# Kernel optimization log

Measured on AMD Instinct MI355X. Metric: run time of the kernel, lower is better.

Reference implementation:

```python
import jax, jax.numpy as jnp
import numpy as np

# ShapeNet category -> contiguous segment range (16 categories, 50 segments)
SEG_LENS = np.array([4, 2, 2, 4, 4, 3, 3, 2, 4, 2, 6, 2, 3, 3, 3, 3], dtype=np.int32)
SHIFTS = np.concatenate([[0], np.cumsum(SEG_LENS)[:-1]]).astype(np.int32)
NUM_CAT = 16
IN_F = 256
MAX_SEG_COUNT = 6   # max len(seg) over categories
MAX_SEG = 49        # max segment id
N_PTS = 32768
BN_EPS = 1e-5


def setup_inputs() -> dict:
    key = jax.random.key(0)
    k1, k2, k3, k4 = jax.random.split(key, 4)
    features = jax.random.normal(k1, (N_PTS, IN_F), dtype=jnp.float32)
    W1 = jax.random.normal(k2, (IN_F, NUM_CAT * IN_F), dtype=jnp.float32) * (1.0 / np.sqrt(IN_F))
    gamma = jnp.ones((NUM_CAT * IN_F,), dtype=jnp.float32)
    beta = jnp.zeros((NUM_CAT * IN_F,), dtype=jnp.float32)
    Wc = jax.random.normal(k3, (NUM_CAT, IN_F, MAX_SEG_COUNT), dtype=jnp.float32) * (1.0 / np.sqrt(IN_F))
    bias = jnp.zeros((MAX_SEG_COUNT,), dtype=jnp.float32)
    cats = jax.random.randint(k4, (N_PTS,), 0, NUM_CAT, dtype=jnp.int32)
    return {
        "features": features, "W1": W1, "gamma": gamma, "beta": beta,
        "Wc": Wc, "bias": bias, "cats": cats,
        "shifts": jnp.asarray(SHIFTS), "seg_lens": jnp.asarray(SEG_LENS),
    }


def reference(features, W1, gamma, beta, Wc, bias, cats, shifts, seg_lens):
    N, F = features.shape
    C, _, S = Wc.shape
    # channel_rasing: Linear(bias=False) -> BatchNorm1d (batch stats) -> LeakyReLU(0.2)
    x = features @ W1                              # [N, C*F]
    mu = x.mean(axis=0)
    var = x.var(axis=0)                            # biased, as BatchNorm
    x = (x - mu) * jax.lax.rsqrt(var + BN_EPS) * gamma + beta
    x = jnp.where(x >= 0, x, 0.2 * x)              # LeakyReLU(0.2); Dropout = identity (eval)
    # UnaryConv: per-category matmul + shared bias -> [C, N, S]
    x = x.reshape(N, C, F)
    feats = jnp.einsum('ncf,cfs->cns', x, Wc) + bias
    # gather the assigned category's logits per point -> [N, S]
    logits = feats[cats, jnp.arange(N)]
    lsm = jax.nn.log_softmax(logits, axis=-1)
    # scatter (expressed as gather) into per-category segment ranges -> [N, MAX_SEG+1]
    sh = shifts[cats]                              # [N]
    ln = seg_lens[cats]                            # [N]
    k = jnp.arange(MAX_SEG + 1, dtype=jnp.int32)   # [50]
    j = k[None, :] - sh[:, None]                   # [N, 50]
    valid = (j >= 0) & (j < ln[:, None])
    jc = jnp.clip(j, 0, S - 1)
    out = jnp.where(valid, jnp.take_along_axis(lsm, jc, axis=1), 0.0)
    return out
```

## Files before the change

kernel.cpp:

```cpp
#include <hip/hip_runtime.h>
#include <hip/hip_bf16.h>
#include <math.h>

#define N_PTS 32768
#define IN_F  256
#define NUM_CAT 16
#define CF    4096
#define NSEG  6
#define OUTK  50
#define BN_EPS 1e-5f

typedef unsigned short u16;
typedef __attribute__((ext_vector_type(8))) short bf16x8;
typedef __attribute__((ext_vector_type(4))) float f32x4;
typedef __attribute__((ext_vector_type(8))) unsigned short u16x8;

#define OFF_G     0u
#define OFF_FBAR  65536u
#define OFF_SCALE 65792u
#define OFF_SHIFT 69888u
#define OFF_INT   73984u
#define OFF_FB    106832u
#define OFF_FBT   4301136u
#define OFF_W1T   8495440u
#define OFF_GP    9019728u
#define IO_COUNTS 0
#define IO_CATOFF 16
#define IO_TILEST 33
#define IO_NTILES 50
#define IO_CURSOR 51
#define IO_ORDER  67

__device__ __forceinline__ void gload_lds16(const void* g, void* l) {
    __builtin_amdgcn_global_load_lds(
        (const __attribute__((address_space(1))) void*)g,
        (__attribute__((address_space(3))) void*)l,
        16, 0, 0);
}
__device__ __forceinline__ u16 f2bf(float f) {
    unsigned int u = __float_as_uint(f);
    return (u16)((u + 0x7FFF + ((u >> 16) & 1)) >> 16);
}
__device__ __forceinline__ float bf2f(u16 h) {
    return __uint_as_float((unsigned int)h << 16);
}

__global__ __launch_bounds__(256) void k0_cvt(const float* __restrict__ F,
                                              u16* __restrict__ Fb,
                                              u16* __restrict__ FbT) {
    const int pb = blockIdx.x >> 2, fb = blockIdx.x & 3;
    const int p0 = pb * 64, f0 = fb * 64;
    const int tid = threadIdx.x;
    __shared__ u16 T[64][72];
    {
        int p = tid >> 2, fq = tid & 3;
        const float* src = &F[(size_t)(p0 + p) * IN_F + f0 + fq * 16];
        u16x8 o0, o1;
        float4 v0 = *(const float4*)&src[0];
        float4 v1 = *(const float4*)&src[4];
        float4 v2 = *(const float4*)&src[8];
        float4 v3 = *(const float4*)&src[12];
        o0[0]=f2bf(v0.x); o0[1]=f2bf(v0.y); o0[2]=f2bf(v0.z); o0[3]=f2bf(v0.w);
        o0[4]=f2bf(v1.x); o0[5]=f2bf(v1.y); o0[6]=f2bf(v1.z); o0[7]=f2bf(v1.w);
        o1[0]=f2bf(v2.x); o1[1]=f2bf(v2.y); o1[2]=f2bf(v2.z); o1[3]=f2bf(v2.w);
        o1[4]=f2bf(v3.x); o1[5]=f2bf(v3.y); o1[6]=f2bf(v3.z); o1[7]=f2bf(v3.w);
        u16* dst = &Fb[(size_t)(p0 + p) * IN_F + f0 + fq * 16];
        *(u16x8*)dst = o0; *(u16x8*)&dst[8] = o1;
        *(u16x8*)&T[p][fq * 16] = o0; *(u16x8*)&T[p][fq * 16 + 8] = o1;
    }
    __syncthreads();
    {
        int f = tid >> 2, pq = tid & 3;
        u16x8 a0, a1;
#pragma unroll
        for (int m = 0; m < 8; m++) { a0[m] = T[pq*16 + m][f]; a1[m] = T[pq*16 + 8 + m][f]; }
        u16* dst = &FbT[(size_t)(f0 + f) * N_PTS + p0 + pq * 16];
        *(u16x8*)dst = a0; *(u16x8*)&dst[8] = a1;
    }
}

__global__ __launch_bounds__(256) void k0b_w1t(const float* __restrict__ W1,
                                               u16* __restrict__ W1T) {
    __shared__ u16 T[64][65];
    const int kb = blockIdx.x & 3, jb = blockIdx.x >> 2;
    const int tid = threadIdx.x;
    {
        int kk = tid >> 2, j4 = (tid & 3) * 16;
        const float* src = &W1[(size_t)(kb * 64 + kk) * CF + jb * 64 + j4];
#pragma unroll
        for (int q = 0; q < 4; q++) {
            float4 v = *(const float4*)&src[q * 4];
            T[kk][j4 + q * 4 + 0] = f2bf(v.x); T[kk][j4 + q * 4 + 1] = f2bf(v.y);
            T[kk][j4 + q * 4 + 2] = f2bf(v.z); T[kk][j4 + q * 4 + 3] = f2bf(v.w);
        }
    }
    __syncthreads();
    {
        int jj = tid >> 2, ks = (tid & 3) * 16;
        int c = jb >> 2, n = (jb & 3) * 64 + jj;
        u16* dst = &W1T[((size_t)(c * 256 + n)) * 256 + kb * 64 + ks];
        u16x8 o0, o1;
#pragma unroll
        for (int m = 0; m < 8; m++) { o0[m] = T[ks + m][jj]; o1[m] = T[ks + 8 + m][jj]; }
        *(u16x8*)dst = o0;
        *(u16x8*)&dst[8] = o1;
    }
}

__global__ __launch_bounds__(256) void k1_gram(const u16* __restrict__ FbT,
                                               float* __restrict__ ws,
                                               int nchunk, int Kc) {
    const int TI[10] = {0,0,0,0,1,1,1,2,2,3};
    const int TJ[10] = {0,1,2,3,1,2,3,2,3,3};
    const int t = blockIdx.x % 10, chunk = blockIdx.x / 10;
    const int i0 = TI[t] * 64, j0 = TJ[t] * 64;
    const int r0 = chunk * Kc;
    const int tid = threadIdx.x;
    const int wv = tid >> 6, ln = tid & 63, g = ln >> 4, r16 = ln & 15;
    __shared__ __align__(16) u16 SA[2][4096];
    __shared__ __align__(16) u16 SB[2][4096];

    const int q0 = wv * 2, q1 = wv * 2 + 1;
    const int u_a = ((q0 * 64 + ln) & 7), row_a = (q0 * 64 + ln) >> 3;
    const int u_b = ((q1 * 64 + ln) & 7), row_b = (q1 * 64 + ln) >> 3;
    const int ka = ((u_a ^ (row_a & 7)) << 3), kb2 = ((u_b ^ (row_b & 7)) << 3);

    f32x4 acc[4];
#pragma unroll
    for (int nt = 0; nt < 4; nt++)
#pragma unroll
        for (int i = 0; i < 4; i++) acc[nt][i] = 0.f;

    const int nslab = Kc >> 6;
#define K1_STAGE(s, b)                                                              \
    {   int p0s = r0 + (s) * 64;                                                    \
        gload_lds16(FbT + (size_t)(i0 + row_a) * N_PTS + p0s + ka,                  \
                    (char*)SA[b] + q0 * 1024);                                      \
        gload_lds16(FbT + (size_t)(i0 + row_b) * N_PTS + p0s + kb2,                 \
                    (char*)SA[b] + q1 * 1024);                                      \
        gload_lds16(FbT + (size_t)(j0 + row_a) * N_PTS + p0s + ka,                  \
                    (char*)SB[b] + q0 * 1024);                                      \
        gload_lds16(FbT + (size_t)(j0 + row_b) * N_PTS + p0s + kb2,                 \
                    (char*)SB[b] + q1 * 1024);                                      \
    }

    K1_STAGE(0, 0);
    __syncthreads();
    for (int s = 0; s < nslab; s++) {
        const int b = s & 1;
        if (s + 1 < nslab) K1_STAGE(s + 1, b ^ 1);
#pragma unroll
        for (int ks = 0; ks < 2; ks++) {
            int ph = (ks * 4 + g) ^ (r16 & 7);
            bf16x8 a = *(const bf16x8*)((const char*)SA[b] + (wv * 16 + r16) * 128 + ph * 16);
#pragma unroll
            for (int nt = 0; nt < 4; nt++) {
                int nB = nt * 16 + r16;
                bf16x8 bb = *(const bf16x8*)((const char*)SB[b] + nB * 128 + ph * 16);
                acc[nt] = __builtin_amdgcn_mfma_f32_16x16x32_bf16(a, bb, acc[nt], 0, 0, 0);
            }
        }
        __syncthreads();
    }
    float* Gp = ws + OFF_GP + (size_t)chunk * 40960 + t * 4096;
#pragma unroll
    for (int nt = 0; nt < 4; nt++)
#pragma unroll
        for (int i = 0; i < 4; i++) {
            int row = wv * 16 + g * 4 + i, col = nt * 16 + r16;
            Gp[row * 64 + col] = acc[nt][i];
        }
}

__global__ __launch_bounds__(256) void k1b_colsum(const u16* __restrict__ FbT,
                                                  float* __restrict__ ws) {
    const int row = blockIdx.x, tid = threadIdx.x;
    const u16* r = FbT + (size_t)row * N_PTS;
    float s = 0.f;
    for (int i = tid * 8; i < N_PTS; i += 2048) {
        u16x8 v = *(const u16x8*)&r[i];
#pragma unroll
        for (int m = 0; m < 8; m++) s += bf2f(v[m]);
    }
#pragma unroll
    for (int off = 32; off >= 1; off >>= 1) s += __shfl_xor(s, off);
    __shared__ float ps[4];
    if ((tid & 63) == 0) ps[tid >> 6] = s;
    __syncthreads();
    if (tid == 0) ws[OFF_FBAR + row] = (ps[0] + ps[1] + ps[2] + ps[3]) * (1.0f / N_PTS);
    if (blockIdx.x == 0 && tid < 16) ((int*)(ws + OFF_INT))[IO_COUNTS + tid] = 0;
}

__global__ __launch_bounds__(256) void k2a_reduce(float* __restrict__ ws, int nchunk) {
    const int TI[10] = {0,0,0,0,1,1,1,2,2,3};
    const int TJ[10] = {0,1,2,3,1,2,3,2,3,3};
    const int e = blockIdx.x * 256 + threadIdx.x;
    const float* p = ws + OFF_GP + e;
    float s = 0.f;
#pragma unroll 8
    for (int c = 0; c < nchunk; c++) s += p[(size_t)c * 40960];
    int t = e >> 12, x = (e >> 6) & 63, y = e & 63;
    int a = TI[t] * 64 + x, b = TJ[t] * 64 + y;
    ws[OFF_G + a * 256 + b] = s;
    ws[OFF_G + b * 256 + a] = s;
}

__global__ __launch_bounds__(256) void k2b_stats(const float* __restrict__ W1,
                                                 const float* __restrict__ gamma,
                                                 const float* __restrict__ beta,
                                                 float* __restrict__ ws) {
    const int tid = threadIdx.x;
    const int j0 = blockIdx.x * 16;
    __shared__ __align__(16) float wl[16][256];
    __shared__ float pw[16][8];
#pragma unroll
    for (int q = 0; q < 4; q++) {
        float4 v = *(const float4*)&W1[(size_t)tid * CF + j0 + q * 4];
        wl[q * 4 + 0][tid] = v.x; wl[q * 4 + 1][tid] = v.y;
        wl[q * 4 + 2][tid] = v.z; wl[q * 4 + 3][tid] = v.w;
    }
    __syncthreads();
    float acc[16];
#pragma unroll
    for (int jj = 0; jj < 16; jj++) acc[jj] = 0.f;
    const float* G = ws + OFF_G;
    for (int b = 0; b < 256; b++) {
        float g = G[b * 256 + tid];
#pragma unroll
        for (int jj = 0; jj < 16; jj++) acc[jj] += g * wl[jj][b];
    }
    float fb = ws[OFF_FBAR + tid];
    const int lane = tid & 63, wave = tid >> 6;
#pragma unroll
    for (int jj = 0; jj < 16; jj++) {
        float v = wl[jj][tid] * acc[jj];
        float m = fb * wl[jj][tid];
#pragma unroll
        for (int off = 32; off >= 1; off >>= 1) {
            v += __shfl_xor(v, off);
            m += __shfl_xor(m, off);
        }
        if (lane == 0) { pw[jj][wave * 2] = v; pw[jj][wave * 2 + 1] = m; }
    }
    __syncthreads();
    if (tid < 16) {
        int jj = tid;
        float v = 0.f, m = 0.f;
        for (int w2 = 0; w2 < 4; w2++) { v += pw[jj][w2 * 2]; m += pw[jj][w2 * 2 + 1]; }
        float mu  = m;
        float var = v * (1.0f / N_PTS) - mu * mu;
        float sc  = gamma[j0 + jj] * rsqrtf(var + BN_EPS);
        float sh  = beta[j0 + jj] - mu * sc;
        ws[OFF_SCALE + j0 + jj] = sc;
        ws[OFF_SHIFT + j0 + jj] = sh;
    }
}

__global__ __launch_bounds__(256) void k3_hist(const int* __restrict__ cats,
                                               float* __restrict__ ws) {
    __shared__ int h[16];
    int tid = threadIdx.x;
    if (tid < 16) h[tid] = 0;
    __syncthreads();
    for (int n = blockIdx.x * 256 + tid; n < N_PTS; n += 64 * 256)
        atomicAdd(&h[cats[n]], 1);
    __syncthreads();
    int* wi = (int*)(ws + OFF_INT);
    if (tid < 16) atomicAdd(&wi[IO_COUNTS + tid], h[tid]);
}

__global__ void k4_prefix(float* __restrict__ ws) {
    int* wi = (int*)(ws + OFF_INT);
    if (threadIdx.x == 0) {
        int co = 0, ts = 0;
        wi[IO_CATOFF] = 0; wi[IO_TILEST] = 0;
        for (int c = 0; c < 16; c++) {
            int cnt = wi[IO_COUNTS + c];
            wi[IO_CURSOR + c] = co;
            co += cnt; ts += (cnt + 63) >> 6;
            wi[IO_CATOFF + c + 1] = co;
            wi[IO_TILEST + c + 1] = ts;
        }
        wi[IO_NTILES] = ts;
    }
}

__global__ __launch_bounds__(256) void k4b_scatter(const int* __restrict__ cats,
                                                   float* __restrict__ ws) {
    int* wi = (int*)(ws + OFF_INT);
    __shared__ int lh[16], lbase[16];
    const int tid = threadIdx.x;
    const int n0 = blockIdx.x * 512;
    if (tid < 16) lh[tid] = 0;
    __syncthreads();
    const int cA = cats[n0 + tid];
    const int cB = cats[n0 + 256 + tid];
    atomicAdd(&lh[cA], 1);
    atomicAdd(&lh[cB], 1);
    __syncthreads();
    if (tid < 16) lbase[tid] = atomicAdd(&wi[IO_CURSOR + tid], lh[tid]);
    __syncthreads();
    if (tid < 16) lh[tid] = 0;
    __syncthreads();
    int rA = atomicAdd(&lh[cA], 1);
    wi[IO_ORDER + lbase[cA] + rA] = n0 + tid;
    int rB = atomicAdd(&lh[cB], 1);
    wi[IO_ORDER + lbase[cB] + rB] = n0 + 256 + tid;
}

__global__ __launch_bounds__(256) void k5_mfma(const u16* __restrict__ Fb,
                                               const u16* __restrict__ W1T,
                                               const float* __restrict__ Wc,
                                               const float* __restrict__ bias,
                                               const int* __restrict__ shifts,
                                               const int* __restrict__ seg_lens,
                                               const float* __restrict__ ws,
                                               float* __restrict__ out) {
    const int* wi = (const int*)(ws + OFF_INT);
    const int t = blockIdx.x;
    if (t >= wi[IO_NTILES]) return;
    int c = 0;
    while (!(t >= wi[IO_TILEST + c] && t < wi[IO_TILEST + c + 1])) c++;
    const int lt = t - wi[IO_TILEST + c];
    const int base = wi[IO_CATOFF + c] + lt * 64;
    const int npts = min(64, wi[IO_COUNTS + c] - lt * 64);
    const int tid = threadIdx.x;
    const int wv = tid >> 6, ln = tid & 63;
    const int g = ln >> 4, r16 = ln & 15;

    __shared__ __align__(16) unsigned char U[32768];
    __shared__ float scl[256], shl[256], wcl[1536];
    __shared__ int plds[64];

    if (tid < 64) plds[tid] = wi[IO_ORDER + base + min(tid, npts - 1)];
    scl[tid] = ws[OFF_SCALE + c * 256 + tid];
    shl[tid] = ws[OFF_SHIFT + c * 256 + tid];
#pragma unroll
    for (int i = 0; i < 6; i++) wcl[tid + i * 256] = Wc[(size_t)c * 1536 + tid + i * 256];
    __syncthreads();

#pragma unroll
    for (int s = 0; s < 8; s++) {
        int flat = s * 256 + tid;
        int pt = flat >> 5, u = flat & 31;
        const u16* src = Fb + (size_t)plds[pt] * 256 + ((u ^ (pt & 7)) << 3);
        gload_lds16(src, U + (size_t)(s * 4 + wv) * 1024);
    }
    __syncthreads();

    const u16* W1Tc = W1T + (size_t)c * 65536;
    const u16* wp0 = W1Tc + (size_t)(wv * 64 +  0 + r16) * 256 + g * 8;
    const u16* wp1 = W1Tc + (size_t)(wv * 64 + 16 + r16) * 256 + g * 8;
    const u16* wp2 = W1Tc + (size_t)(wv * 64 + 32 + r16) * 256 + g * 8;
    const u16* wp3 = W1Tc + (size_t)(wv * 64 + 48 + r16) * 256 + g * 8;

    f32x4 acc[4][4];
#pragma unroll
    for (int mt = 0; mt < 4; mt++)
#pragma unroll
        for (int nt = 0; nt < 4; nt++)
#pragma unroll
            for (int i = 0; i < 4; i++) acc[mt][nt][i] = 0.f;

    bf16x8 bf[2][4];
    bf[0][0] = *(const bf16x8*)(wp0);
    bf[0][1] = *(const bf16x8*)(wp1);
    bf[0][2] = *(const bf16x8*)(wp2);
    bf[0][3] = *(const bf16x8*)(wp3);

#pragma unroll
    for (int kc = 0; kc < 8; kc++) {
        if (kc < 7) {
            bf[(kc + 1) & 1][0] = *(const bf16x8*)(wp0 + (kc + 1) * 32);
            bf[(kc + 1) & 1][1] = *(const bf16x8*)(wp1 + (kc + 1) * 32);
            bf[(kc + 1) & 1][2] = *(const bf16x8*)(wp2 + (kc + 1) * 32);
            bf[(kc + 1) & 1][3] = *(const bf16x8*)(wp3 + (kc + 1) * 32);
        }
        bf16x8 af[4];
#pragma unroll
        for (int mt = 0; mt < 4; mt++) {
            int row = mt * 16 + r16;
            int phys = (kc * 4 + g) ^ (row & 7);
            af[mt] = *(const bf16x8*)(U + (size_t)row * 512 + phys * 16);
        }
#pragma unroll
        for (int mt = 0; mt < 4; mt++)
#pragma unroll
            for (int nt = 0; nt < 4; nt++)
                acc[mt][nt] = __builtin_amdgcn_mfma_f32_16x16x32_bf16(
                    af[mt], bf[kc & 1][nt], acc[mt][nt], 0, 0, 0);
    }

    __syncthreads();
    float* red2 = (float*)U;
#pragma unroll
    for (int mt = 0; mt < 4; mt++)
#pragma unroll
        for (int i = 0; i < 4; i++) {
            float pl[6] = {0.f, 0.f, 0.f, 0.f, 0.f, 0.f};
#pragma unroll
            for (int nt = 0; nt < 4; nt++) {
                int col = wv * 64 + nt * 16 + r16;
                float x = acc[mt][nt][i] * scl[col] + shl[col];
                x = (x >= 0.f) ? x : 0.2f * x;
#pragma unroll
                for (int s = 0; s < 6; s++) pl[s] += x * wcl[col * 6 + s];
            }
#pragma unroll
            for (int s = 0; s < 6; s++) {
                pl[s] += __shfl_xor(pl[s], 1);
                pl[s] += __shfl_xor(pl[s], 2);
                pl[s] += __shfl_xor(pl[s], 4);
                pl[s] += __shfl_xor(pl[s], 8);
            }
            if (r16 == 0) {
                int pt = mt * 16 + g * 4 + i;
#pragma unroll
                for (int s = 0; s < 6; s++) red2[(pt * 4 + wv) * 6 + s] = pl[s];
            }
        }
    __syncthreads();

    if (tid < 64 && tid < npts) {
        float lg[6];
#pragma unroll
        for (int s = 0; s < 6; s++) lg[s] = bias[s];
#pragma unroll
        for (int w = 0; w < 4; w++)
#pragma unroll
            for (int s = 0; s < 6; s++) lg[s] += red2[(tid * 4 + w) * 6 + s];
        float mx = lg[0];
#pragma unroll
        for (int s = 1; s < 6; s++) mx = fmaxf(mx, lg[s]);
        float se = 0.f;
#pragma unroll
        for (int s = 0; s < 6; s++) se += expf(lg[s] - mx);
        float lse = mx + logf(se);
        const int pid = plds[tid];
        const int sh = shifts[c], ln2 = seg_lens[c];
        float* orow = out + (size_t)pid * OUTK;
        for (int k = 0; k < OUTK; k++) {
            int j = k - sh;
            orow[k] = (j >= 0 && j < ln2) ? (lg[j] - lse) : 0.f;
        }
    }
}

extern "C" void kernel_launch(void* const* d_in, const int* in_sizes, int n_in,
                              void* d_out, int out_size, void* d_ws, size_t ws_size,
                              hipStream_t stream) {
    const float* F      = (const float*)d_in[0];
    const float* W1     = (const float*)d_in[1];
    const float* gamma  = (const float*)d_in[2];
    const float* beta   = (const float*)d_in[3];
    const float* Wc     = (const float*)d_in[4];
    const float* bias   = (const float*)d_in[5];
    const int*  cats    = (const int*)d_in[6];
    const int*  shifts  = (const int*)d_in[7];
    const int*  seglens = (const int*)d_in[8];
    float* out = (float*)d_out;
    float* ws  = (float*)d_ws;
    u16* Fb  = (u16*)(ws + OFF_FB);
    u16* FbT = (u16*)(ws + OFF_FBT);
    u16* W1T = (u16*)(ws + OFF_W1T);

    int nchunk = 64;
    if (ws_size < ((size_t)OFF_GP + 40960ull * 64) * 4) nchunk = 32;
    if (ws_size < ((size_t)OFF_GP + 40960ull * 32) * 4) nchunk = 16;
    const int Kc = N_PTS / nchunk;

    hipLaunchKernelGGL(k0_cvt,      dim3(2048), dim3(256), 0, stream, F, Fb, FbT);
    hipLaunchKernelGGL(k0b_w1t,     dim3(256),  dim3(256), 0, stream, W1, W1T);
    hipLaunchKernelGGL(k1_gram,     dim3(10 * nchunk), dim3(256), 0, stream, FbT, ws, nchunk, Kc);
    hipLaunchKernelGGL(k1b_colsum,  dim3(256),  dim3(256), 0, stream, FbT, ws);
    hipLaunchKernelGGL(k2a_reduce,  dim3(160),  dim3(256), 0, stream, ws, nchunk);
    hipLaunchKernelGGL(k2b_stats,   dim3(256),  dim3(256), 0, stream, W1, gamma, beta, ws);
    hipLaunchKernelGGL(k3_hist,     dim3(64),   dim3(256), 0, stream, cats, ws);
    hipLaunchKernelGGL(k4_prefix,   dim3(1),    dim3(64),  0, stream, ws);
    hipLaunchKernelGGL(k4b_scatter, dim3(64),   dim3(256), 0, stream, cats, ws);
    hipLaunchKernelGGL(k5_mfma,     dim3(528),  dim3(256), 0, stream,
                       Fb, W1T, Wc, bias, shifts, seglens, ws, out);
}
```

Before: 115.3 us.

## Stage W1 tiles through LDS with double-buffered async loads in 512-thread GEMM

The main MFMA kernel moves to 512 threads (8 waves, each covering 32 output columns) and stages the category's W1 slice into swizzled LDS in four K-quarters. It double-buffers them with direct global-to-LDS loads and explicit vmcnt waits so that loads overlap compute. Tile-to-category lookup is precomputed in the prefix kernel as a packed table, replacing the per-block linear search. The cost is 96KB+ of LDS per block, which limits occupancy to about one block per CU, plus a larger cross-wave reduction.

```diff
diff --git a/kernel.cpp b/kernel.cpp
--- a/kernel.cpp
+++ b/kernel.cpp
@@ -20,16 +20,17 @@
 #define OFF_SCALE 65792u
 #define OFF_SHIFT 69888u
 #define OFF_INT   73984u
-#define OFF_FB    106832u
-#define OFF_FBT   4301136u
-#define OFF_W1T   8495440u
-#define OFF_GP    9019728u
+#define OFF_FB    107424u
+#define OFF_FBT   4301728u
+#define OFF_W1T   8496032u
+#define OFF_GP    9020320u
 #define IO_COUNTS 0
 #define IO_CATOFF 16
 #define IO_TILEST 33
 #define IO_NTILES 50
 #define IO_CURSOR 51
 #define IO_ORDER  67
+#define IO_TILECAT 32835
 
 __device__ __forceinline__ void gload_lds16(const void* g, void* l) {
     __builtin_amdgcn_global_load_lds(
@@ -277,7 +278,13 @@
         for (int c = 0; c < 16; c++) {
             int cnt = wi[IO_COUNTS + c];
             wi[IO_CURSOR + c] = co;
-            co += cnt; ts += (cnt + 63) >> 6;
+            int nt = (cnt + 63) >> 6;
+            for (int lt = 0; lt < nt; lt++) {
+                int npts = min(64, cnt - lt * 64);
+                int b = co + lt * 64;
+                wi[IO_TILECAT + ts + lt] = c | ((npts - 1) << 4) | (b << 10);
+            }
+            co += cnt; ts += nt;
             wi[IO_CATOFF + c + 1] = co;
             wi[IO_TILEST + c + 1] = ts;
         }
@@ -308,7 +315,7 @@
     wi[IO_ORDER + lbase[cB] + rB] = n0 + 256 + tid;
 }
 
-__global__ __launch_bounds__(256) void k5_mfma(const u16* __restrict__ Fb,
+__global__ __launch_bounds__(512) void k5_mfma(const u16* __restrict__ Fb,
                                                const u16* __restrict__ W1T,
                                                const float* __restrict__ Wc,
                                                const float* __restrict__ bias,
@@ -319,77 +326,101 @@
     const int* wi = (const int*)(ws + OFF_INT);
     const int t = blockIdx.x;
     if (t >= wi[IO_NTILES]) return;
-    int c = 0;
-    while (!(t >= wi[IO_TILEST + c] && t < wi[IO_TILEST + c + 1])) c++;
-    const int lt = t - wi[IO_TILEST + c];
-    const int base = wi[IO_CATOFF + c] + lt * 64;
-    const int npts = min(64, wi[IO_COUNTS + c] - lt * 64);
+    const unsigned info = (unsigned)wi[IO_TILECAT + t];
+    const int c    = info & 15;
+    const int npts = ((info >> 4) & 63) + 1;
+    const int base = info >> 10;
     const int tid = threadIdx.x;
     const int wv = tid >> 6, ln = tid & 63;
     const int g = ln >> 4, r16 = ln & 15;
 
-    __shared__ __align__(16) unsigned char U[32768];
+    __shared__ __align__(16) unsigned char U[98304];
     __shared__ float scl[256], shl[256], wcl[1536];
     __shared__ int plds[64];
 
     if (tid < 64) plds[tid] = wi[IO_ORDER + base + min(tid, npts - 1)];
-    scl[tid] = ws[OFF_SCALE + c * 256 + tid];
-    shl[tid] = ws[OFF_SHIFT + c * 256 + tid];
-#pragma unroll
-    for (int i = 0; i < 6; i++) wcl[tid + i * 256] = Wc[(size_t)c * 1536 + tid + i * 256];
-    __syncthreads();
-
-#pragma unroll
-    for (int s = 0; s < 8; s++) {
-        int flat = s * 256 + tid;
+    if (tid < 256) {
+        scl[tid] = ws[OFF_SCALE + c * 256 + tid];
+        shl[tid] = ws[OFF_SHIFT + c * 256 + tid];
+    }
+#pragma unroll
+    for (int i = 0; i < 3; i++) wcl[tid + i * 512] = Wc[(size_t)c * 1536 + tid + i * 512];
+    __syncthreads();
+
+    const u16* W1Tc = W1T + (size_t)c * 65536;
+
+#define STAGE_WQ(q, b)                                                             \
+    {                                                                              \
+        _Pragma("unroll")                                                          \
+        for (int i2 = 0; i2 < 4; i2++) {                                           \
+            int f = i2 * 64 + ln;                                                  \
+            int r = f >> 3, u = f & 7;                                             \
+            int n = wv * 32 + r;                                                   \
+            const u16* src = W1Tc + (size_t)n * 256 + (q) * 64 + ((u ^ (n & 7)) << 3); \
+            gload_lds16(src, U + 32768 + (b) * 32768 + wv * 4096 + i2 * 1024);     \
+        }                                                                          \
+    }
+
+    STAGE_WQ(0, 0);
+    STAGE_WQ(1, 1);
+#pragma unroll
+    for (int s = 0; s < 4; s++) {
+        int flat = (wv * 4 + s) * 64 + ln;
         int pt = flat >> 5, u = flat & 31;
         const u16* src = Fb + (size_t)plds[pt] * 256 + ((u ^ (pt & 7)) << 3);
-        gload_lds16(src, U + (size_t)(s * 4 + wv) * 1024);
-    }
-    __syncthreads();
-
-    const u16* W1Tc = W1T + (size_t)c * 65536;
-    const u16* wp0 = W1Tc + (size_t)(wv * 64 +  0 + r16) * 256 + g * 8;
-    const u16* wp1 = W1Tc + (size_t)(wv * 64 + 16 + r16) * 256 + g * 8;
-    const u16* wp2 = W1Tc + (size_t)(wv * 64 + 32 + r16) * 256 + g * 8;
-    const u16* wp3 = W1Tc + (size_t)(wv * 64 + 48 + r16) * 256 + g * 8;
-
-    f32x4 acc[4][4];
+        gload_lds16(src, U + (size_t)(wv * 4 + s) * 1024);
+    }
+    __syncthreads();
+
+    f32x4 acc[4][2];
 #pragma unroll
     for (int mt = 0; mt < 4; mt++)
 #pragma unroll
-        for (int nt = 0; nt < 4; nt++)
+        for (int nt = 0; nt < 2; nt++)
 #pragma unroll
             for (int i = 0; i < 4; i++) acc[mt][nt][i] = 0.f;
 
-    bf16x8 bf[2][4];
-    bf[0][0] = *(const bf16x8*)(wp0);
-    bf[0][1] = *(const bf16x8*)(wp1);
-    bf[0][2] = *(const bf16x8*)(wp2);
-    bf[0][3] = *(const bf16x8*)(wp3);
-
-#pragma unroll
-    for (int kc = 0; kc < 8; kc++) {
-        if (kc < 7) {
-            bf[(kc + 1) & 1][0] = *(const bf16x8*)(wp0 + (kc + 1) * 32);
-            bf[(kc + 1) & 1][1] = *(const bf16x8*)(wp1 + (kc + 1) * 32);
-            bf[(kc + 1) & 1][2] = *(const bf16x8*)(wp2 + (kc + 1) * 32);
-            bf[(kc + 1) & 1][3] = *(const bf16x8*)(wp3 + (kc + 1) * 32);
-        }
-        bf16x8 af[4];
-#pragma unroll
-        for (int mt = 0; mt < 4; mt++) {
-            int row = mt * 16 + r16;
-            int phys = (kc * 4 + g) ^ (row & 7);
-            af[mt] = *(const bf16x8*)(U + (size_t)row * 512 + phys * 16);
-        }
-#pragma unroll
-        for (int mt = 0; mt < 4; mt++)
-#pragma unroll
-            for (int nt = 0; nt < 4; nt++)
-                acc[mt][nt] = __builtin_amdgcn_mfma_f32_16x16x32_bf16(
-                    af[mt], bf[kc & 1][nt], acc[mt][nt], 0, 0, 0);
-    }
+#define COMP_Q(q, b)                                                               \
+    {                                                                              \
+        _Pragma("unroll")                                                          \
+        for (int h = 0; h < 2; h++) {                                              \
+            const int kc = (q) * 2 + h;                                            \
+            bf16x8 af[4], bfr[2];                                                  \
+            _Pragma("unroll")                                                      \
+            for (int mt = 0; mt < 4; mt++) {                                       \
+                int row = mt * 16 + r16;                                           \
+                int phys = (kc * 4 + g) ^ (row & 7);                               \
+                af[mt] = *(const bf16x8*)(U + (size_t)row * 512 + phys * 16);      \
+            }                                                                      \
+            _Pragma("unroll")                                                      \
+            for (int nt = 0; nt < 2; nt++) {                                       \
+                int n = wv * 32 + nt * 16 + r16;                                   \
+                int r = nt * 16 + r16;                                             \
+                int phys = (h * 4 + g) ^ (n & 7);                                  \
+                bfr[nt] = *(const bf16x8*)(U + 32768 + (b) * 32768                 \
+                                           + wv * 4096 + r * 128 + phys * 16);    \
+            }                                                                      \
+            _Pragma("unroll")                                                      \
+            for (int mt = 0; mt < 4; mt++)                                         \
+                _Pragma("unroll")                                                  \
+                for (int nt = 0; nt < 2; nt++)                                     \
+                    acc[mt][nt] = __builtin_amdgcn_mfma_f32_16x16x32_bf16(         \
+                        af[mt], bfr[nt], acc[mt][nt], 0, 0, 0);                    \
+        }                                                                          \
+    }
+
+    COMP_Q(0, 0);
+    __builtin_amdgcn_sched_barrier(0);
+    STAGE_WQ(2, 0);
+    COMP_Q(1, 1);
+    __builtin_amdgcn_sched_barrier(0);
+    STAGE_WQ(3, 1);
+    asm volatile("s_waitcnt vmcnt(4)" ::: "memory");
+    __builtin_amdgcn_sched_barrier(0);
+    COMP_Q(2, 0);
+    asm volatile("s_waitcnt vmcnt(0)" ::: "memory");
+    __builtin_amdgcn_sched_barrier(0);
+    COMP_Q(3, 1);
 
     __syncthreads();
     float* red2 = (float*)U;
@@ -399,8 +430,8 @@
         for (int i = 0; i < 4; i++) {
             float pl[6] = {0.f, 0.f, 0.f, 0.f, 0.f, 0.f};
 #pragma unroll
-            for (int nt = 0; nt < 4; nt++) {
-                int col = wv * 64 + nt * 16 + r16;
+            for (int nt = 0; nt < 2; nt++) {
+                int col = wv * 32 + nt * 16 + r16;
                 float x = acc[mt][nt][i] * scl[col] + shl[col];
                 x = (x >= 0.f) ? x : 0.2f * x;
 #pragma unroll
@@ -416,7 +447,7 @@
             if (r16 == 0) {
                 int pt = mt * 16 + g * 4 + i;
 #pragma unroll
-                for (int s = 0; s < 6; s++) red2[(pt * 4 + wv) * 6 + s] = pl[s];
+                for (int s = 0; s < 6; s++) red2[(pt * 8 + wv) * 6 + s] = pl[s];
             }
         }
     __syncthreads();
@@ -426,9 +457,9 @@
 #pragma unroll
         for (int s = 0; s < 6; s++) lg[s] = bias[s];
 #pragma unroll
-        for (int w = 0; w < 4; w++)
-#pragma unroll
-            for (int s = 0; s < 6; s++) lg[s] += red2[(tid * 4 + w) * 6 + s];
+        for (int w = 0; w < 8; w++)
+#pragma unroll
+            for (int s = 0; s < 6; s++) lg[s] += red2[(tid * 8 + w) * 6 + s];
         float mx = lg[0];
 #pragma unroll
         for (int s = 1; s < 6; s++) mx = fmaxf(mx, lg[s]);
@@ -478,6 +509,6 @@
     hipLaunchKernelGGL(k3_hist,     dim3(64),   dim3(256), 0, stream, cats, ws);
     hipLaunchKernelGGL(k4_prefix,   dim3(1),    dim3(64),  0, stream, ws);
     hipLaunchKernelGGL(k4b_scatter, dim3(64),   dim3(256), 0, stream, cats, ws);
-    hipLaunchKernelGGL(k5_mfma,     dim3(528),  dim3(256), 0, stream,
+    hipLaunchKernelGGL(k5_mfma,     dim3(528),  dim3(512), 0, stream,
                        Fb, W1T, Wc, bias, shifts, seglens, ws, out);
 }
```

New measurement: 151.0 us. 1.31x slower.

## Stage per-category W1 slice in LDS and stream 128-point tiles in chunks

Applied to the files above, without the earlier changes.

The main MFMA kernel now loads the whole 256x256 bf16 W1 slice for a category into LDS (128 KB) once per block. It then streams 128 points in 16-point double-buffered chunks with 512 threads, instead of reading W1 from global memory for every 64-point tile. Tile-to-category lookup moves into a precomputed packed table built by the prefix kernel, and the output is written cooperatively. The stats kernel processes 32 columns per block. This halves the number of W1 reads but uses very large LDS per block, so only one block fits per CU, and it adds a sync per chunk.

```diff
diff --git a/kernel.cpp b/kernel.cpp
--- a/kernel.cpp
+++ b/kernel.cpp
@@ -20,16 +20,17 @@
 #define OFF_SCALE 65792u
 #define OFF_SHIFT 69888u
 #define OFF_INT   73984u
-#define OFF_FB    106832u
-#define OFF_FBT   4301136u
-#define OFF_W1T   8495440u
-#define OFF_GP    9019728u
+#define OFF_FB    107424u
+#define OFF_FBT   4301728u
+#define OFF_W1T   8496032u
+#define OFF_GP    9020320u
 #define IO_COUNTS 0
 #define IO_CATOFF 16
 #define IO_TILEST 33
 #define IO_NTILES 50
 #define IO_CURSOR 51
 #define IO_ORDER  67
+#define IO_TILECAT 32835
 
 __device__ __forceinline__ void gload_lds16(const void* g, void* l) {
     __builtin_amdgcn_global_load_lds(
@@ -210,29 +211,29 @@
                                                  const float* __restrict__ beta,
                                                  float* __restrict__ ws) {
     const int tid = threadIdx.x;
-    const int j0 = blockIdx.x * 16;
-    __shared__ __align__(16) float wl[16][256];
-    __shared__ float pw[16][8];
-#pragma unroll
-    for (int q = 0; q < 4; q++) {
+    const int j0 = blockIdx.x * 32;
+    __shared__ __align__(16) float wl[32][256];
+    __shared__ float pw[32][8];
+#pragma unroll
+    for (int q = 0; q < 8; q++) {
         float4 v = *(const float4*)&W1[(size_t)tid * CF + j0 + q * 4];
         wl[q * 4 + 0][tid] = v.x; wl[q * 4 + 1][tid] = v.y;
         wl[q * 4 + 2][tid] = v.z; wl[q * 4 + 3][tid] = v.w;
     }
     __syncthreads();
-    float acc[16];
-#pragma unroll
-    for (int jj = 0; jj < 16; jj++) acc[jj] = 0.f;
+    float acc[32];
+#pragma unroll
+    for (int jj = 0; jj < 32; jj++) acc[jj] = 0.f;
     const float* G = ws + OFF_G;
     for (int b = 0; b < 256; b++) {
         float g = G[b * 256 + tid];
 #pragma unroll
-        for (int jj = 0; jj < 16; jj++) acc[jj] += g * wl[jj][b];
+        for (int jj = 0; jj < 32; jj++) acc[jj] += g * wl[jj][b];
     }
     float fb = ws[OFF_FBAR + tid];
     const int lane = tid & 63, wave = tid >> 6;
 #pragma unroll
-    for (int jj = 0; jj < 16; jj++) {
+    for (int jj = 0; jj < 32; jj++) {
         float v = wl[jj][tid] * acc[jj];
         float m = fb * wl[jj][tid];
 #pragma unroll
@@ -243,7 +244,7 @@
         if (lane == 0) { pw[jj][wave * 2] = v; pw[jj][wave * 2 + 1] = m; }
     }
     __syncthreads();
-    if (tid < 16) {
+    if (tid < 32) {
         int jj = tid;
         float v = 0.f, m = 0.f;
         for (int w2 = 0; w2 < 4; w2++) { v += pw[jj][w2 * 2]; m += pw[jj][w2 * 2 + 1]; }
@@ -277,7 +278,13 @@
         for (int c = 0; c < 16; c++) {
             int cnt = wi[IO_COUNTS + c];
             wi[IO_CURSOR + c] = co;
-            co += cnt; ts += (cnt + 63) >> 6;
+            int nt = (cnt + 127) >> 7;
+            for (int lt = 0; lt < nt; lt++) {
+                int npts = min(128, cnt - lt * 128);
+                int b = co + lt * 128;
+                wi[IO_TILECAT + ts + lt] = c | ((npts - 1) << 4) | (b << 11);
+            }
+            co += cnt; ts += nt;
             wi[IO_CATOFF + c + 1] = co;
             wi[IO_TILEST + c + 1] = ts;
         }
@@ -308,7 +315,7 @@
     wi[IO_ORDER + lbase[cB] + rB] = n0 + 256 + tid;
 }
 
-__global__ __launch_bounds__(256) void k5_mfma(const u16* __restrict__ Fb,
+__global__ __launch_bounds__(512) void k5_mfma(const u16* __restrict__ Fb,
                                                const u16* __restrict__ W1T,
                                                const float* __restrict__ Wc,
                                                const float* __restrict__ bias,
@@ -319,129 +326,122 @@
     const int* wi = (const int*)(ws + OFF_INT);
     const int t = blockIdx.x;
     if (t >= wi[IO_NTILES]) return;
-    int c = 0;
-    while (!(t >= wi[IO_TILEST + c] && t < wi[IO_TILEST + c + 1])) c++;
-    const int lt = t - wi[IO_TILEST + c];
-    const int base = wi[IO_CATOFF + c] + lt * 64;
-    const int npts = min(64, wi[IO_COUNTS + c] - lt * 64);
+    const unsigned info = (unsigned)wi[IO_TILECAT + t];
+    const int c    = info & 15;
+    const int npts = ((info >> 4) & 127) + 1;
+    const int base = info >> 11;
     const int tid = threadIdx.x;
     const int wv = tid >> 6, ln = tid & 63;
     const int g = ln >> 4, r16 = ln & 15;
 
-    __shared__ __align__(16) unsigned char U[32768];
-    __shared__ float scl[256], shl[256], wcl[1536];
-    __shared__ int plds[64];
-
-    if (tid < 64) plds[tid] = wi[IO_ORDER + base + min(tid, npts - 1)];
-    scl[tid] = ws[OFF_SCALE + c * 256 + tid];
-    shl[tid] = ws[OFF_SHIFT + c * 256 + tid];
-#pragma unroll
-    for (int i = 0; i < 6; i++) wcl[tid + i * 256] = Wc[(size_t)c * 1536 + tid + i * 256];
-    __syncthreads();
-
-#pragma unroll
-    for (int s = 0; s < 8; s++) {
-        int flat = s * 256 + tid;
-        int pt = flat >> 5, u = flat & 31;
-        const u16* src = Fb + (size_t)plds[pt] * 256 + ((u ^ (pt & 7)) << 3);
-        gload_lds16(src, U + (size_t)(s * 4 + wv) * 1024);
-    }
-    __syncthreads();
+    __shared__ __align__(16) u16 Wl[65536];
+    __shared__ __align__(16) u16 Fl[2][4096];
+    __shared__ float red[16][8][6];
+    __shared__ int plds[128];
+
+    if (tid < 128) plds[tid] = wi[IO_ORDER + base + min(tid, npts - 1)];
 
     const u16* W1Tc = W1T + (size_t)c * 65536;
-    const u16* wp0 = W1Tc + (size_t)(wv * 64 +  0 + r16) * 256 + g * 8;
-    const u16* wp1 = W1Tc + (size_t)(wv * 64 + 16 + r16) * 256 + g * 8;
-    const u16* wp2 = W1Tc + (size_t)(wv * 64 + 32 + r16) * 256 + g * 8;
-    const u16* wp3 = W1Tc + (size_t)(wv * 64 + 48 + r16) * 256 + g * 8;
-
-    f32x4 acc[4][4];
-#pragma unroll
-    for (int mt = 0; mt < 4; mt++)
-#pragma unroll
-        for (int nt = 0; nt < 4; nt++)
-#pragma unroll
-            for (int i = 0; i < 4; i++) acc[mt][nt][i] = 0.f;
-
-    bf16x8 bf[2][4];
-    bf[0][0] = *(const bf16x8*)(wp0);
-    bf[0][1] = *(const bf16x8*)(wp1);
-    bf[0][2] = *(const bf16x8*)(wp2);
-    bf[0][3] = *(const bf16x8*)(wp3);
-
-#pragma unroll
-    for (int kc = 0; kc < 8; kc++) {
-        if (kc < 7) {
-            bf[(kc + 1) & 1][0] = *(const bf16x8*)(wp0 + (kc + 1) * 32);
-            bf[(kc + 1) & 1][1] = *(const bf16x8*)(wp1 + (kc + 1) * 32);
-            bf[(kc + 1) & 1][2] = *(const bf16x8*)(wp2 + (kc + 1) * 32);
-            bf[(kc + 1) & 1][3] = *(const bf16x8*)(wp3 + (kc + 1) * 32);
-        }
-        bf16x8 af[4];
-#pragma unroll
-        for (int mt = 0; mt < 4; mt++) {
-            int row = mt * 16 + r16;
-            int phys = (kc * 4 + g) ^ (row & 7);
-            af[mt] = *(const bf16x8*)(U + (size_t)row * 512 + phys * 16);
-        }
-#pragma unroll
-        for (int mt = 0; mt < 4; mt++)
-#pragma unroll
-            for (int nt = 0; nt < 4; nt++)
-                acc[mt][nt] = __builtin_amdgcn_mfma_f32_16x16x32_bf16(
-                    af[mt], bf[kc & 1][nt], acc[mt][nt], 0, 0, 0);
-    }
-
-    __syncthreads();
-    float* red2 = (float*)U;
-#pragma unroll
-    for (int mt = 0; mt < 4; mt++)
+#pragma unroll
+    for (int i = 0; i < 16; i++) {
+        int flat = i * 512 + tid;
+        int n = flat >> 5, u = flat & 31;
+        const u16* src = W1Tc + (size_t)n * 256 + ((u ^ (n & 7)) << 3);
+        gload_lds16(src, (char*)Wl + i * 8192 + wv * 1024);
+    }
+
+    const int col0 = wv * 32 + r16, col1 = col0 + 16;
+    const float sc0 = ws[OFF_SCALE + c * 256 + col0];
+    const float sc1 = ws[OFF_SCALE + c * 256 + col1];
+    const float sh0 = ws[OFF_SHIFT + c * 256 + col0];
+    const float sh1 = ws[OFF_SHIFT + c * 256 + col1];
+    float wc0[6], wc1[6];
+#pragma unroll
+    for (int s = 0; s < 6; s++) {
+        wc0[s] = Wc[(size_t)c * 1536 + col0 * 6 + s];
+        wc1[s] = Wc[(size_t)c * 1536 + col1 * 6 + s];
+    }
+    const float biasj = ((tid & 7) < 6) ? bias[tid & 7] : 0.f;
+    const int shc = shifts[c], lnc = seg_lens[c];
+
+    __syncthreads();
+
+    const int fpt = tid >> 5, fu = tid & 31;
+    u16x8 pf = *(const u16x8*)(Fb + (size_t)plds[fpt] * 256 + fu * 8);
+    const int fdst = fpt * 256 + ((fu ^ (fpt & 7)) << 3);
+    const int r7 = r16 & 7;
+
+    for (int ck = 0; ck < 8; ck++) {
+        const int cur = ck & 1;
+        *(u16x8*)(Fl[cur] + fdst) = pf;
+        __syncthreads();
+        if (ck < 7)
+            pf = *(const u16x8*)(Fb + (size_t)plds[(ck + 1) * 16 + fpt] * 256 + fu * 8);
+
+        f32x4 acc0 = {0.f, 0.f, 0.f, 0.f}, acc1 = {0.f, 0.f, 0.f, 0.f};
+#pragma unroll
+        for (int kc = 0; kc < 8; kc++) {
+            const int ph = ((kc * 4 + g) ^ r7) * 16;
+            bf16x8 af = *(const bf16x8*)((const char*)Fl[cur] + r16 * 512 + ph);
+            bf16x8 b0 = *(const bf16x8*)((const char*)Wl + col0 * 512 + ph);
+            bf16x8 b1 = *(const bf16x8*)((const char*)Wl + col1 * 512 + ph);
+            acc0 = __builtin_amdgcn_mfma_f32_16x16x32_bf16(af, b0, acc0, 0, 0, 0);
+            acc1 = __builtin_amdgcn_mfma_f32_16x16x32_bf16(af, b1, acc1, 0, 0, 0);
+        }
+
+        float pl[4][6];
 #pragma unroll
         for (int i = 0; i < 4; i++) {
-            float pl[6] = {0.f, 0.f, 0.f, 0.f, 0.f, 0.f};
-#pragma unroll
-            for (int nt = 0; nt < 4; nt++) {
-                int col = wv * 64 + nt * 16 + r16;
-                float x = acc[mt][nt][i] * scl[col] + shl[col];
-                x = (x >= 0.f) ? x : 0.2f * x;
-#pragma unroll
-                for (int s = 0; s < 6; s++) pl[s] += x * wcl[col * 6 + s];
+            float x0 = acc0[i] * sc0 + sh0;  x0 = (x0 >= 0.f) ? x0 : 0.2f * x0;
+            float x1 = acc1[i] * sc1 + sh1;  x1 = (x1 >= 0.f) ? x1 : 0.2f * x1;
+#pragma unroll
+            for (int s = 0; s < 6; s++) pl[i][s] = x0 * wc0[s] + x1 * wc1[s];
+        }
+#pragma unroll
+        for (int i = 0; i < 4; i++)
+#pragma unroll
+            for (int s = 0; s < 6; s++) {
+                pl[i][s] += __shfl_xor(pl[i][s], 1);
+                pl[i][s] += __shfl_xor(pl[i][s], 2);
+                pl[i][s] += __shfl_xor(pl[i][s], 4);
+                pl[i][s] += __shfl_xor(pl[i][s], 8);
             }
-#pragma unroll
-            for (int s = 0; s < 6; s++) {
-                pl[s] += __shfl_xor(pl[s], 1);
-                pl[s] += __shfl_xor(pl[s], 2);
-                pl[s] += __shfl_xor(pl[s], 4);
-                pl[s] += __shfl_xor(pl[s], 8);
+        if (r16 == 0) {
+#pragma unroll
+            for (int i = 0; i < 4; i++)
+#pragma unroll
+                for (int s = 0; s < 6; s++) red[g * 4 + i][wv][s] = pl[i][s];
+        }
+        __syncthreads();
+
+        if (tid < 128) {
+            const int lpt = tid >> 3, j = tid & 7;
+            float v = -1e30f;
+            if (j < 6) {
+                v = biasj;
+#pragma unroll
+                for (int w = 0; w < 8; w++) v += red[lpt][w][j];
             }
-            if (r16 == 0) {
-                int pt = mt * 16 + g * 4 + i;
-#pragma unroll
-                for (int s = 0; s < 6; s++) red2[(pt * 4 + wv) * 6 + s] = pl[s];
+            float mx = v;
+            mx = fmaxf(mx, __shfl_xor(mx, 1));
+            mx = fmaxf(mx, __shfl_xor(mx, 2));
+            mx = fmaxf(mx, __shfl_xor(mx, 4));
+            float e = (j < 6) ? expf(v - mx) : 0.f;
+            float se = e;
+            se += __shfl_xor(se, 1);
+            se += __shfl_xor(se, 2);
+            se += __shfl_xor(se, 4);
+            float lse = mx + logf(se);
+            const int gpt = ck * 16 + lpt;
+            if (gpt < npts) {
+                if (j < 6) red[lpt][0][j] = v - lse;
+                const int pid = plds[gpt];
+                float* orow = out + (size_t)pid * OUTK;
+                for (int k = j; k < OUTK; k += 8) {
+                    int jj = k - shc;
+                    orow[k] = (jj >= 0 && jj < lnc) ? red[lpt][0][jj] : 0.f;
+                }
             }
-        }
-    __syncthreads();
-
-    if (tid < 64 && tid < npts) {
-        float lg[6];
-#pragma unroll
-        for (int s = 0; s < 6; s++) lg[s] = bias[s];
-#pragma unroll
-        for (int w = 0; w < 4; w++)
-#pragma unroll
-            for (int s = 0; s < 6; s++) lg[s] += red2[(tid * 4 + w) * 6 + s];
-        float mx = lg[0];
-#pragma unroll
-        for (int s = 1; s < 6; s++) mx = fmaxf(mx, lg[s]);
-        float se = 0.f;
-#pragma unroll
-        for (int s = 0; s < 6; s++) se += expf(lg[s] - mx);
-        float lse = mx + logf(se);
-        const int pid = plds[tid];
-        const int sh = shifts[c], ln2 = seg_lens[c];
-        float* orow = out + (size_t)pid * OUTK;
-        for (int k = 0; k < OUTK; k++) {
-            int j = k - sh;
-            orow[k] = (j >= 0 && j < ln2) ? (lg[j] - lse) : 0.f;
         }
     }
 }
@@ -474,10 +474,10 @@
     hipLaunchKernelGGL(k1_gram,     dim3(10 * nchunk), dim3(256), 0, stream, FbT, ws, nchunk, Kc);
     hipLaunchKernelGGL(k1b_colsum,  dim3(256),  dim3(256), 0, stream, FbT, ws);
     hipLaunchKernelGGL(k2a_reduce,  dim3(160),  dim3(256), 0, stream, ws, nchunk);
-    hipLaunchKernelGGL(k2b_stats,   dim3(256),  dim3(256), 0, stream, W1, gamma, beta, ws);
+    hipLaunchKernelGGL(k2b_stats,   dim3(128),  dim3(256), 0, stream, W1, gamma, beta, ws);
     hipLaunchKernelGGL(k3_hist,     dim3(64),   dim3(256), 0, stream, cats, ws);
     hipLaunchKernelGGL(k4_prefix,   dim3(1),    dim3(64),  0, stream, ws);
     hipLaunchKernelGGL(k4b_scatter, dim3(64),   dim3(256), 0, stream, cats, ws);
-    hipLaunchKernelGGL(k5_mfma,     dim3(528),  dim3(256), 0, stream,
+    hipLaunchKernelGGL(k5_mfma,     dim3(272),  dim3(512), 0, stream,
                        Fb, W1T, Wc, bias, shifts, seglens, ws, out);
 }
```

After: 187.5 us. 1.63x slower.
